# Kernel tuning notes

Hardware: AMD Instinct MI355X
Metric: run time of the kernel (lower is better)

## Reference

```python
import jax, jax.numpy as jnp
import numpy as np
import math

H, W = 1024, 1280
NUM_CLASSES = 81  # 80 foreground + background
CENTER_VAR, SIZE_VAR = 0.1, 0.2
CONF_THR, NMS_THR = 0.01, 0.45
PRE_NMS_K, MAX_DET = 400, 100

def make_priors():
    strides_x = [32, 64, 128, 213, 320]
    strides_y = [32, 64, 128, 256, 512]
    fmx = [int(W / s) for s in strides_x]
    fmy = [int(H / s) for s in strides_y]
    expand = H / 256.0
    mins = [10 * expand, 62 * expand, 114 * expand, 166 * expand, 218 * expand]
    maxs = [62 * expand, 114 * expand, 166 * expand, 218 * expand, 270 * expand]
    ars = [[2, 3], [2, 3], [2, 3], [2], [2]]
    pri = []
    for k in range(5):
        for i in range(fmy[k]):
            for j in range(fmx[k]):
                cx = (j + 0.5) / fmx[k]
                cy = (i + 0.5) / fmy[k]
                pri.append([cx, cy, mins[k] / W, mins[k] / H])
                s = math.sqrt(mins[k] * maxs[k])
                pri.append([cx, cy, s / W, s / H])
                for r in ars[k]:
                    sr = math.sqrt(r)
                    pri.append([cx, cy, mins[k] * sr / W, mins[k] / sr / H])
                    pri.append([cx, cy, mins[k] / sr / W, mins[k] * sr / H])
    return np.clip(np.asarray(pri, np.float32), 0.0, 1.0)  # [P,4] center form

def setup_inputs():
    key = jax.random.key(0)
    k1, k2 = jax.random.split(key)
    pri = jnp.asarray(make_priors())  # [10208, 4]
    P = pri.shape[0]
    return {
        "cls_logits": jax.random.normal(k1, (32, P, NUM_CLASSES), jnp.float32),
        "bbox_pred": jax.random.normal(k2, (32, P, 4), jnp.float32) * 0.5,
        "priors": pri,
    }

def _decode(loc, priors):
    # convert_locations_to_boxes: center-form decode with variances
    c = loc[..., :2] * CENTER_VAR * priors[..., 2:] + priors[..., :2]
    s = jnp.exp(loc[..., 2:] * SIZE_VAR) * priors[..., 2:]
    # center_form_to_corner_form
    return jnp.concatenate([c - s * 0.5, c + s * 0.5], axis=-1)

def _iou(a, b):
    lt = jnp.maximum(a[:, None, :2], b[None, :, :2])
    rb = jnp.minimum(a[:, None, 2:], b[None, :, 2:])
    wh = jnp.clip(rb - lt, 0.0)
    inter = wh[..., 0] * wh[..., 1]
    ar = (a[:, 2] - a[:, 0]) * (a[:, 3] - a[:, 1])
    br = (b[:, 2] - b[:, 0]) * (b[:, 3] - b[:, 1])
    return inter / (ar[:, None] + br[None, :] - inter + 1e-9)

def _post_one(scores, boxes):
    # scores: [P, C] softmax probs, boxes: [P, 4] corner form in [0,1]
    C = scores.shape[1]
    fg = scores[:, 1:]  # drop background
    bx = boxes * jnp.asarray([W, H, W, H], boxes.dtype)  # scale to image coords
    topv, topi = jax.lax.top_k(fg.reshape(-1), PRE_NMS_K)  # pre-NMS candidates
    prior_idx = topi // (C - 1)
    cls = topi % (C - 1) + 1
    cb = bx[prior_idx]  # [K,4]
    # class-aware (batched) NMS: offset boxes by class so classes never overlap
    off = cls.astype(bx.dtype)[:, None] * float(max(H, W) + 1)
    ob = cb + off
    iou = _iou(ob, ob)  # [K,K]
    keep0 = topv > CONF_THR
    idx = jnp.arange(PRE_NMS_K)
    def body(keep, i):
        sup = (iou[i] > NMS_THR) & (idx > i) & keep[i]
        return keep & ~sup, None
    keep, _ = jax.lax.scan(body, keep0, jnp.arange(PRE_NMS_K))
    sc = jnp.where(keep, topv, 0.0)
    fv, fi = jax.lax.top_k(sc, MAX_DET)
    return cb[fi], cls[fi], fv  # boxes [100,4], labels [100], scores [100]

def reference(cls_logits, bbox_pred, priors):
    scores = jax.nn.softmax(cls_logits, axis=2)  # [B,P,C]
    boxes = _decode(bbox_pred, priors)           # [B,P,4]
    return jax.vmap(_post_one)(scores, boxes)
```

## Files before the change

### kernel.cpp

```cpp
#include <hip/hip_runtime.h>


#define BATCH   32
#define NCLS    81
#define CM1     80
#define KPRE    400
#define MAXDET  100
#define NBINS   4096
#define CAP     32768
#define THRESH  0.06f
#define CONFT   0.01f
#define NMST    0.45f
#define OFFMUL  1281.0f
#define WD      1280.0f
#define HT      1024.0f

#define SPB     256

#define OFF_CNT   0u
#define ZERO_BYTES 128u
#define OFF_CAND  1024u
#define OFF_TOPV  8389632u
#define OFF_CLS   8440832u
#define OFF_BOX   8492032u
#define OFF_SUP   8696832u

__global__ __launch_bounds__(256, 3) void k_score(const float* __restrict__ logits,
                                                  unsigned int* __restrict__ cnt,
                                                  uint2* __restrict__ cand, int P) {
    int b = blockIdx.y;
    int p0 = blockIdx.x * SPB;
    int npb = min(SPB, P - p0);
    int t = threadIdx.x;
    __shared__ unsigned int blk_cnt, blk_base;

    if (t == 0) blk_cnt = 0;
    __syncthreads();

    bool active = (t < npb);
    float x[NCLS];
    float mx = 0.f, s = 0.f, thr = 0.f;
    unsigned int mycnt = 0, myoff = 0;
    if (active) {
        const float* __restrict__ row = logits + ((size_t)b * P + p0 + t) * NCLS;
        #pragma unroll
        for (int c = 0; c < NCLS; ++c) x[c] = row[c];

        float m0 = x[0], m1 = x[1], m2 = x[2], m3 = x[3];
        #pragma unroll
        for (int c = 4; c + 3 < NCLS; c += 4) {
            m0 = fmaxf(m0, x[c]);     m1 = fmaxf(m1, x[c + 1]);
            m2 = fmaxf(m2, x[c + 2]); m3 = fmaxf(m3, x[c + 3]);
        }
        mx = fmaxf(fmaxf(fmaxf(m0, m1), fmaxf(m2, m3)), x[NCLS - 1]);
        s = 0.0f;
        #pragma unroll
        for (int c = 0; c < NCLS; ++c) s = __fadd_rn(s, expf(__fsub_rn(x[c], mx)));
        thr = mx + logf(THRESH * s) - 1e-3f;
        #pragma unroll
        for (int c = 1; c < NCLS; ++c) mycnt += (x[c] > thr) ? 1u : 0u;
        if (mycnt) myoff = atomicAdd(&blk_cnt, mycnt);
    }
    __syncthreads();
    if (t == 0) blk_base = atomicAdd(&cnt[b], blk_cnt);
    __syncthreads();

    if (active && mycnt) {
        unsigned int pos = blk_base + myoff;
        unsigned int baseIdx = (unsigned int)(p0 + t) * CM1;
        #pragma unroll
        for (int c = 1; c < NCLS; ++c) {
            float xv = x[c];
            if (xv > thr) {
                float pr = __fdiv_rn(expf(__fsub_rn(xv, mx)), s);
                if (pos < CAP)
                    cand[(size_t)b * CAP + pos] = make_uint2(__float_as_uint(pr),
                                                             baseIdx + (unsigned)(c - 1));
                pos++;
            }
        }
    }
}

__global__ __launch_bounds__(512) void k_select(const unsigned int* __restrict__ cnt,
                                                const uint2* __restrict__ cand,
                                                const float* __restrict__ bbox,
                                                const float* __restrict__ priors,
                                                float* __restrict__ topv,
                                                unsigned int* __restrict__ clsA,
                                                float* __restrict__ boxA, int P) {
    int b = blockIdx.x;
    int tid = threadIdx.x;
    __shared__ unsigned int lh[NBINS];
    __shared__ unsigned long long keys[2048];
    __shared__ unsigned int sh_bstar, sh_M;

    for (int i = tid; i < NBINS; i += 512) lh[i] = 0u;
    if (tid == 0) sh_M = 0;
    __syncthreads();

    unsigned int n = min(cnt[b], (unsigned)CAP);
    for (unsigned int j = tid; j < n; j += 512) {
        unsigned int bits = cand[(size_t)b * CAP + j].x;
        atomicAdd(&lh[bits >> 19], 1u);
    }
    __syncthreads();

    if (tid < 64) {
        int lane = tid;
        unsigned int bsum = 0;
        for (int m = 0; m < 64; ++m) { int mm = (m + lane) & 63; bsum += lh[lane * 64 + mm]; }
        unsigned int S = bsum;
        for (int off = 1; off < 64; off <<= 1) {
            unsigned int o = __shfl(S, min(lane + off, 63));
            if (lane + off < 64) S += o;
        }
        unsigned int Sn = __shfl(S, min(lane + 1, 63)); if (lane == 63) Sn = 0;
        bool cond = (S >= KPRE) && (Sn < KPRE);
        unsigned long long bal = __ballot(cond);
        int Ls = (bal == 0) ? 0 : (__ffsll((long long)bal) - 1);
        unsigned int coarse = __shfl(Sn, Ls);
        unsigned int T = lh[Ls * 64 + lane];
        for (int off = 1; off < 64; off <<= 1) {
            unsigned int o = __shfl(T, min(lane + off, 63));
            if (lane + off < 64) T += o;
        }
        unsigned int Tn = __shfl(T, min(lane + 1, 63)); if (lane == 63) Tn = 0;
        bool cond2 = (coarse + T >= KPRE) && (coarse + Tn < KPRE);
        unsigned long long bal2 = __ballot(cond2);
        int Ms = (bal2 == 0) ? 0 : (__ffsll((long long)bal2) - 1);
        if (lane == 0) sh_bstar = (unsigned)(Ls * 64 + Ms);
    }
    __syncthreads();
    unsigned int bstar = sh_bstar;

    for (unsigned int j = tid; j < n; j += 512) {
        uint2 cd = cand[(size_t)b * CAP + j];
        if ((cd.x >> 19) >= bstar) {
            unsigned int pos = atomicAdd(&sh_M, 1u);
            if (pos < 2048) keys[pos] = ((unsigned long long)cd.x << 32) | (unsigned int)(~cd.y);
        }
    }
    __syncthreads();
    unsigned int M = min(sh_M, 2048u);
    unsigned int S2 = 512; while (S2 < M) S2 <<= 1;
    for (unsigned int i = M + tid; i < S2; i += 512) keys[i] = 0ull;
    __syncthreads();

    for (unsigned int k = 2; k <= S2; k <<= 1) {
        for (unsigned int j = k >> 1; j > 0; j >>= 1) {
            for (unsigned int i = tid; i < S2; i += 512) {
                unsigned int pi = i ^ j;
                if (pi > i) {
                    unsigned long long a = keys[i], bb = keys[pi];
                    bool sw = ((i & k) == 0) ? (a < bb) : (a > bb);
                    if (sw) { keys[i] = bb; keys[pi] = a; }
                }
            }
            __syncthreads();
        }
    }

    for (int k2 = tid; k2 < KPRE; k2 += 512) {
        unsigned long long key = keys[k2];
        unsigned int bits = (unsigned int)(key >> 32);
        unsigned int idx = ~((unsigned int)key);
        float val, x1, y1, x2, y2; unsigned int cc;
        if (bits == 0u) { val = 0.f; x1 = y1 = x2 = y2 = 0.f; cc = 0u; }
        else {
            val = __uint_as_float(bits);
            unsigned int prior = idx / CM1;
            cc = idx - prior * CM1 + 1u;
            const float* lp = bbox + ((size_t)b * P + prior) * 4;
            const float* pp = priors + (size_t)prior * 4;
            float cx = __fadd_rn(__fmul_rn(__fmul_rn(lp[0], 0.1f), pp[2]), pp[0]);
            float cy = __fadd_rn(__fmul_rn(__fmul_rn(lp[1], 0.1f), pp[3]), pp[1]);
            float sw = __fmul_rn(expf(__fmul_rn(lp[2], 0.2f)), pp[2]);
            float sh = __fmul_rn(expf(__fmul_rn(lp[3], 0.2f)), pp[3]);
            x1 = __fmul_rn(__fsub_rn(cx, __fmul_rn(sw, 0.5f)), WD);
            y1 = __fmul_rn(__fsub_rn(cy, __fmul_rn(sh, 0.5f)), HT);
            x2 = __fmul_rn(__fadd_rn(cx, __fmul_rn(sw, 0.5f)), WD);
            y2 = __fmul_rn(__fadd_rn(cy, __fmul_rn(sh, 0.5f)), HT);
        }
        size_t o = (size_t)b * KPRE + k2;
        topv[o] = val; clsA[o] = cc;
        boxA[o * 4 + 0] = x1; boxA[o * 4 + 1] = y1; boxA[o * 4 + 2] = x2; boxA[o * 4 + 3] = y2;
    }
}

__global__ __launch_bounds__(512) void k_iou(const float* __restrict__ boxA,
                                             const unsigned int* __restrict__ clsA,
                                             unsigned long long* __restrict__ sup) {
    int b = blockIdx.x;
    int w = blockIdx.y;
    int tid = threadIdx.x;
    __shared__ float ob[KPRE][4];
    const float4* box4 = (const float4*)boxA;
    for (int k = tid; k < KPRE; k += 512) {
        size_t o = (size_t)b * KPRE + k;
        float4 bx = box4[o];
        float off = __fmul_rn((float)clsA[o], OFFMUL);
        ob[k][0] = __fadd_rn(bx.x, off);
        ob[k][1] = __fadd_rn(bx.y, off);
        ob[k][2] = __fadd_rn(bx.z, off);
        ob[k][3] = __fadd_rn(bx.w, off);
    }
    __syncthreads();
    int i = tid;
    if (i >= KPRE) return;
    float a0 = ob[i][0], a1 = ob[i][1], a2 = ob[i][2], a3 = ob[i][3];
    float ar = __fmul_rn(__fsub_rn(a2, a0), __fsub_rn(a3, a1));
    unsigned long long m = 0ull;
    int jmax = min(64, KPRE - w * 64);
    for (int jb = 0; jb < jmax; ++jb) {
        int j = w * 64 + jb;
        float ltx = fmaxf(a0, ob[j][0]), lty = fmaxf(a1, ob[j][1]);
        float rbx = fminf(a2, ob[j][2]), rby = fminf(a3, ob[j][3]);
        float wd = fmaxf(__fsub_rn(rbx, ltx), 0.0f);
        float ht = fmaxf(__fsub_rn(rby, lty), 0.0f);
        float inter = __fmul_rn(wd, ht);
        float br = __fmul_rn(__fsub_rn(ob[j][2], ob[j][0]), __fsub_rn(ob[j][3], ob[j][1]));
        float den = __fadd_rn(__fsub_rn(__fadd_rn(ar, br), inter), 1e-9f);
        float iou = __fdiv_rn(inter, den);
        if (j > i && iou > NMST) m |= (1ull << jb);
    }
    sup[((size_t)b * KPRE + i) * 7 + w] = m;
}

__global__ __launch_bounds__(128) void k_nms(const unsigned long long* __restrict__ sup,
                                             const float* __restrict__ topv,
                                             const unsigned int* __restrict__ clsA,
                                             const float* __restrict__ boxA,
                                             float* __restrict__ out) {
    int b = blockIdx.x;
    int tid = threadIdx.x;
    __shared__ unsigned long long ls[KPRE * 7];
    __shared__ float tv[KPRE];
    __shared__ unsigned long long keepw[7];
    for (int w = tid; w < KPRE * 7; w += 128) ls[w] = sup[(size_t)b * KPRE * 7 + w];
    for (int k = tid; k < KPRE; k += 128) tv[k] = topv[(size_t)b * KPRE + k];
    if (tid < 7) keepw[tid] = 0ull;
    __syncthreads();
    for (int k = tid; k < KPRE; k += 128)
        if (tv[k] > CONFT) atomicOr(&keepw[k >> 6], 1ull << (k & 63));
    __syncthreads();

    if (tid < 64) {
        unsigned long long q0 = keepw[0], q1 = keepw[1], q2 = keepw[2], q3 = keepw[3],
                           q4 = keepw[4], q5 = keepw[5], q6 = keepw[6];
        unsigned long long rb[4][7];
        #pragma unroll
        for (int d = 0; d < 4; ++d) {
            #pragma unroll
            for (int w2 = 0; w2 < 7; ++w2) rb[d][w2] = ls[(unsigned)(d * 7 + w2)];
        }
#define SCANW(W, QW, NB)                                                          \
        for (int b4 = 0; b4 < NB; b4 += 4) {                                      \
            _Pragma("unroll")                                                     \
            for (int u = 0; u < 4; ++u) {                                         \
                int k = W * 64 + b4 + u;                                          \
                unsigned long long msk =                                          \
                    ((QW >> (b4 + u)) & 1ull) ? ~0ull : 0ull;                     \
                q0 &= ~(rb[u][0] & msk); q1 &= ~(rb[u][1] & msk);                 \
                q2 &= ~(rb[u][2] & msk); q3 &= ~(rb[u][3] & msk);                 \
                q4 &= ~(rb[u][4] & msk); q5 &= ~(rb[u][5] & msk);                 \
                q6 &= ~(rb[u][6] & msk);                                          \
                if (k + 4 < KPRE) {                                               \
                    _Pragma("unroll")                                             \
                    for (int w2 = 0; w2 < 7; ++w2)                                \
                        rb[u][w2] = ls[(unsigned)((k + 4) * 7 + w2)];             \
                }                                                                 \
            }                                                                     \
        }
        SCANW(0, q0, 64) SCANW(1, q1, 64) SCANW(2, q2, 64) SCANW(3, q3, 64)
        SCANW(4, q4, 64) SCANW(5, q5, 64) SCANW(6, q6, 16)
#undef SCANW
        if (tid == 0) {
            keepw[0] = q0; keepw[1] = q1; keepw[2] = q2; keepw[3] = q3;
            keepw[4] = q4; keepw[5] = q5; keepw[6] = q6;
        }
    }
    __syncthreads();

    int tot = 0;
    for (int t = 0; t < 7; ++t) tot += __popcll(keepw[t]);
    for (int k = tid; k < KPRE; k += 128) {
        int w = k >> 6, bi = k & 63;
        unsigned long long kw = keepw[w];
        int before = __popcll(kw & ((1ull << bi) - 1ull));
        for (int t = 0; t < w; ++t) before += __popcll(keepw[t]);
        bool kept = (kw >> bi) & 1ull;
        int rank = kept ? before : (tot + (k - before));
        if (rank < MAXDET) {
            size_t so = (size_t)b * KPRE + k;
            size_t dof = (size_t)b * MAXDET + rank;
            out[dof * 4 + 0] = boxA[so * 4 + 0];
            out[dof * 4 + 1] = boxA[so * 4 + 1];
            out[dof * 4 + 2] = boxA[so * 4 + 2];
            out[dof * 4 + 3] = boxA[so * 4 + 3];
            out[(size_t)BATCH * MAXDET * 4 + dof] = (float)clsA[so];
            out[(size_t)BATCH * MAXDET * 5 + dof] = kept ? tv[k] : 0.0f;
        }
    }
}

extern "C" void kernel_launch(void* const* d_in, const int* in_sizes, int n_in,
                              void* d_out, int out_size, void* d_ws, size_t ws_size,
                              hipStream_t stream) {
    (void)n_in; (void)out_size; (void)ws_size;
    const float* logits = (const float*)d_in[0];
    const float* bbox   = (const float*)d_in[1];
    const float* priors = (const float*)d_in[2];
    int P = in_sizes[2] / 4;

    char* ws = (char*)d_ws;
    unsigned int* cnt  = (unsigned int*)(ws + OFF_CNT);
    uint2* cand        = (uint2*)(ws + OFF_CAND);
    float* topv        = (float*)(ws + OFF_TOPV);
    unsigned int* clsA = (unsigned int*)(ws + OFF_CLS);
    float* boxA        = (float*)(ws + OFF_BOX);
    unsigned long long* sup = (unsigned long long*)(ws + OFF_SUP);

    hipMemsetAsync(ws, 0, ZERO_BYTES, stream);

    dim3 g1((P + SPB - 1) / SPB, BATCH);
    k_score<<<g1, 256, 0, stream>>>(logits, cnt, cand, P);
    k_select<<<BATCH, 512, 0, stream>>>(cnt, cand, bbox, priors, topv, clsA, boxA, P);
    k_iou<<<dim3(BATCH, 7), 512, 0, stream>>>(boxA, clsA, sup);
    k_nms<<<BATCH, 128, 0, stream>>>(sup, topv, clsA, boxA, (float*)d_out);
}
```

Before: 269.1 us.

## Fuse IoU and NMS kernels via last-block counter; refine histogram bins

Merges the IoU mask kernel and the NMS scan kernel into one launch. A per-batch atomic counter lets the last of the seven blocks run the greedy scan, which removes one kernel launch and its gap. The select histogram now bins on exponent plus mantissa bits, giving finer resolution near the threshold so fewer candidates survive into the sort. The candidate loops are also unrolled four ways. In exchange it relies on threadfence ordering, and the NMS block now carries the larger shared-memory footprint across all 512 threads.

Result: slower. 302.4 us (+12.4%).

```diff
diff --git a/kernel.cpp b/kernel.cpp
--- a/kernel.cpp
+++ b/kernel.cpp
@@ -18,12 +18,19 @@
 #define SPB     256
 
 #define OFF_CNT   0u
-#define ZERO_BYTES 128u
+#define OFF_DONE  128u
+#define ZERO_BYTES 256u
 #define OFF_CAND  1024u
 #define OFF_TOPV  8389632u
 #define OFF_CLS   8440832u
 #define OFF_BOX   8492032u
 #define OFF_SUP   8696832u
+
+__device__ __forceinline__ int binof(unsigned int bits) {
+    int e = (int)(bits >> 23);
+    int k = (e - 122) * 512 + (int)((bits >> 14) & 0x1FF);
+    return max(0, min(k, NBINS - 1));
+}
 
 __global__ __launch_bounds__(256, 3) void k_score(const float* __restrict__ logits,
                                                   unsigned int* __restrict__ cnt,
@@ -100,9 +107,17 @@
     __syncthreads();
 
     unsigned int n = min(cnt[b], (unsigned)CAP);
-    for (unsigned int j = tid; j < n; j += 512) {
-        unsigned int bits = cand[(size_t)b * CAP + j].x;
-        atomicAdd(&lh[bits >> 19], 1u);
+    const uint2* cb = cand + (size_t)b * CAP;
+    {
+        unsigned int j = tid;
+        for (; j + 1536 < n; j += 2048) {
+            uint2 c0 = cb[j], c1 = cb[j + 512], c2 = cb[j + 1024], c3 = cb[j + 1536];
+            atomicAdd(&lh[binof(c0.x)], 1u);
+            atomicAdd(&lh[binof(c1.x)], 1u);
+            atomicAdd(&lh[binof(c2.x)], 1u);
+            atomicAdd(&lh[binof(c3.x)], 1u);
+        }
+        for (; j < n; j += 512) atomicAdd(&lh[binof(cb[j].x)], 1u);
     }
     __syncthreads();
 
@@ -132,13 +147,35 @@
         if (lane == 0) sh_bstar = (unsigned)(Ls * 64 + Ms);
     }
     __syncthreads();
-    unsigned int bstar = sh_bstar;
-
-    for (unsigned int j = tid; j < n; j += 512) {
-        uint2 cd = cand[(size_t)b * CAP + j];
-        if ((cd.x >> 19) >= bstar) {
-            unsigned int pos = atomicAdd(&sh_M, 1u);
-            if (pos < 2048) keys[pos] = ((unsigned long long)cd.x << 32) | (unsigned int)(~cd.y);
+    int bstar = (int)sh_bstar;
+
+    {
+        unsigned int j = tid;
+        for (; j + 1536 < n; j += 2048) {
+            uint2 c0 = cb[j], c1 = cb[j + 512], c2 = cb[j + 1024], c3 = cb[j + 1536];
+            if (binof(c0.x) >= bstar) {
+                unsigned int pos = atomicAdd(&sh_M, 1u);
+                if (pos < 2048) keys[pos] = ((unsigned long long)c0.x << 32) | (unsigned int)(~c0.y);
+            }
+            if (binof(c1.x) >= bstar) {
+                unsigned int pos = atomicAdd(&sh_M, 1u);
+                if (pos < 2048) keys[pos] = ((unsigned long long)c1.x << 32) | (unsigned int)(~c1.y);
+            }
+            if (binof(c2.x) >= bstar) {
+                unsigned int pos = atomicAdd(&sh_M, 1u);
+                if (pos < 2048) keys[pos] = ((unsigned long long)c2.x << 32) | (unsigned int)(~c2.y);
+            }
+            if (binof(c3.x) >= bstar) {
+                unsigned int pos = atomicAdd(&sh_M, 1u);
+                if (pos < 2048) keys[pos] = ((unsigned long long)c3.x << 32) | (unsigned int)(~c3.y);
+            }
+        }
+        for (; j < n; j += 512) {
+            uint2 cd = cb[j];
+            if (binof(cd.x) >= bstar) {
+                unsigned int pos = atomicAdd(&sh_M, 1u);
+                if (pos < 2048) keys[pos] = ((unsigned long long)cd.x << 32) | (unsigned int)(~cd.y);
+            }
         }
     }
     __syncthreads();
@@ -188,13 +225,17 @@
     }
 }
 
-__global__ __launch_bounds__(512) void k_iou(const float* __restrict__ boxA,
-                                             const unsigned int* __restrict__ clsA,
-                                             unsigned long long* __restrict__ sup) {
+__global__ __launch_bounds__(512) void k_iou_nms(const float* __restrict__ boxA,
+                                                 const unsigned int* __restrict__ clsA,
+                                                 const float* __restrict__ topv,
+                                                 unsigned long long* __restrict__ sup,
+                                                 unsigned int* __restrict__ done,
+                                                 float* __restrict__ out) {
     int b = blockIdx.x;
     int w = blockIdx.y;
     int tid = threadIdx.x;
     __shared__ float ob[KPRE][4];
+    __shared__ unsigned int is_last;
     const float4* box4 = (const float4*)boxA;
     for (int k = tid; k < KPRE; k += 512) {
         size_t o = (size_t)b * KPRE + k;
@@ -207,41 +248,43 @@
     }
     __syncthreads();
     int i = tid;
-    if (i >= KPRE) return;
-    float a0 = ob[i][0], a1 = ob[i][1], a2 = ob[i][2], a3 = ob[i][3];
-    float ar = __fmul_rn(__fsub_rn(a2, a0), __fsub_rn(a3, a1));
-    unsigned long long m = 0ull;
-    int jmax = min(64, KPRE - w * 64);
-    for (int jb = 0; jb < jmax; ++jb) {
-        int j = w * 64 + jb;
-        float ltx = fmaxf(a0, ob[j][0]), lty = fmaxf(a1, ob[j][1]);
-        float rbx = fminf(a2, ob[j][2]), rby = fminf(a3, ob[j][3]);
-        float wd = fmaxf(__fsub_rn(rbx, ltx), 0.0f);
-        float ht = fmaxf(__fsub_rn(rby, lty), 0.0f);
-        float inter = __fmul_rn(wd, ht);
-        float br = __fmul_rn(__fsub_rn(ob[j][2], ob[j][0]), __fsub_rn(ob[j][3], ob[j][1]));
-        float den = __fadd_rn(__fsub_rn(__fadd_rn(ar, br), inter), 1e-9f);
-        float iou = __fdiv_rn(inter, den);
-        if (j > i && iou > NMST) m |= (1ull << jb);
-    }
-    sup[((size_t)b * KPRE + i) * 7 + w] = m;
-}
-
-__global__ __launch_bounds__(128) void k_nms(const unsigned long long* __restrict__ sup,
-                                             const float* __restrict__ topv,
-                                             const unsigned int* __restrict__ clsA,
-                                             const float* __restrict__ boxA,
-                                             float* __restrict__ out) {
-    int b = blockIdx.x;
-    int tid = threadIdx.x;
+    if (i < KPRE) {
+        float a0 = ob[i][0], a1 = ob[i][1], a2 = ob[i][2], a3 = ob[i][3];
+        float ar = __fmul_rn(__fsub_rn(a2, a0), __fsub_rn(a3, a1));
+        unsigned long long m = 0ull;
+        int jmax = min(64, KPRE - w * 64);
+        for (int jb = 0; jb < jmax; ++jb) {
+            int j = w * 64 + jb;
+            float ltx = fmaxf(a0, ob[j][0]), lty = fmaxf(a1, ob[j][1]);
+            float rbx = fminf(a2, ob[j][2]), rby = fminf(a3, ob[j][3]);
+            float wd = fmaxf(__fsub_rn(rbx, ltx), 0.0f);
+            float ht = fmaxf(__fsub_rn(rby, lty), 0.0f);
+            float inter = __fmul_rn(wd, ht);
+            float br = __fmul_rn(__fsub_rn(ob[j][2], ob[j][0]), __fsub_rn(ob[j][3], ob[j][1]));
+            float den = __fadd_rn(__fsub_rn(__fadd_rn(ar, br), inter), 1e-9f);
+            float iou = __fdiv_rn(inter, den);
+            if (j > i && iou > NMST) m |= (1ull << jb);
+        }
+        sup[((size_t)b * KPRE + i) * 7 + w] = m;
+    }
+    __threadfence();
+    __syncthreads();
+    if (tid == 0) {
+        unsigned int old = atomicAdd(&done[b], 1u);
+        is_last = (old == 6u) ? 1u : 0u;
+    }
+    __syncthreads();
+    if (!is_last) return;
+    __threadfence();
+
     __shared__ unsigned long long ls[KPRE * 7];
     __shared__ float tv[KPRE];
     __shared__ unsigned long long keepw[7];
-    for (int w = tid; w < KPRE * 7; w += 128) ls[w] = sup[(size_t)b * KPRE * 7 + w];
-    for (int k = tid; k < KPRE; k += 128) tv[k] = topv[(size_t)b * KPRE + k];
+    for (int q = tid; q < KPRE * 7; q += 512) ls[q] = sup[(size_t)b * KPRE * 7 + q];
+    for (int k = tid; k < KPRE; k += 512) tv[k] = topv[(size_t)b * KPRE + k];
     if (tid < 7) keepw[tid] = 0ull;
     __syncthreads();
-    for (int k = tid; k < KPRE; k += 128)
+    for (int k = tid; k < KPRE; k += 512)
         if (tv[k] > CONFT) atomicOr(&keepw[k >> 6], 1ull << (k & 63));
     __syncthreads();
 
@@ -258,17 +301,17 @@
         for (int b4 = 0; b4 < NB; b4 += 4) {                                      \
             _Pragma("unroll")                                                     \
             for (int u = 0; u < 4; ++u) {                                         \
-                int k = W * 64 + b4 + u;                                          \
+                int kk = W * 64 + b4 + u;                                         \
                 unsigned long long msk =                                          \
                     ((QW >> (b4 + u)) & 1ull) ? ~0ull : 0ull;                     \
                 q0 &= ~(rb[u][0] & msk); q1 &= ~(rb[u][1] & msk);                 \
                 q2 &= ~(rb[u][2] & msk); q3 &= ~(rb[u][3] & msk);                 \
                 q4 &= ~(rb[u][4] & msk); q5 &= ~(rb[u][5] & msk);                 \
                 q6 &= ~(rb[u][6] & msk);                                          \
-                if (k + 4 < KPRE) {                                               \
+                if (kk + 4 < KPRE) {                                              \
                     _Pragma("unroll")                                             \
                     for (int w2 = 0; w2 < 7; ++w2)                                \
-                        rb[u][w2] = ls[(unsigned)((k + 4) * 7 + w2)];             \
+                        rb[u][w2] = ls[(unsigned)((kk + 4) * 7 + w2)];            \
                 }                                                                 \
             }                                                                     \
         }
@@ -283,12 +326,12 @@
     __syncthreads();
 
     int tot = 0;
-    for (int t = 0; t < 7; ++t) tot += __popcll(keepw[t]);
-    for (int k = tid; k < KPRE; k += 128) {
-        int w = k >> 6, bi = k & 63;
-        unsigned long long kw = keepw[w];
+    for (int t2 = 0; t2 < 7; ++t2) tot += __popcll(keepw[t2]);
+    for (int k = tid; k < KPRE; k += 512) {
+        int w2 = k >> 6, bi = k & 63;
+        unsigned long long kw = keepw[w2];
         int before = __popcll(kw & ((1ull << bi) - 1ull));
-        for (int t = 0; t < w; ++t) before += __popcll(keepw[t]);
+        for (int t2 = 0; t2 < w2; ++t2) before += __popcll(keepw[t2]);
         bool kept = (kw >> bi) & 1ull;
         int rank = kept ? before : (tot + (k - before));
         if (rank < MAXDET) {
@@ -315,6 +358,7 @@
 
     char* ws = (char*)d_ws;
     unsigned int* cnt  = (unsigned int*)(ws + OFF_CNT);
+    unsigned int* done = (unsigned int*)(ws + OFF_DONE);
     uint2* cand        = (uint2*)(ws + OFF_CAND);
     float* topv        = (float*)(ws + OFF_TOPV);
     unsigned int* clsA = (unsigned int*)(ws + OFF_CLS);
@@ -326,6 +370,5 @@
     dim3 g1((P + SPB - 1) / SPB, BATCH);
     k_score<<<g1, 256, 0, stream>>>(logits, cnt, cand, P);
     k_select<<<BATCH, 512, 0, stream>>>(cnt, cand, bbox, priors, topv, clsA, boxA, P);
-    k_iou<<<dim3(BATCH, 7), 512, 0, stream>>>(boxA, clsA, sup);
-    k_nms<<<BATCH, 128, 0, stream>>>(sup, topv, clsA, boxA, (float*)d_out);
-}
+    k_iou_nms<<<dim3(BATCH, 7), 512, 0, stream>>>(boxA, clsA, topv, sup, done, (float*)d_out);
+}
```
